# Kernel optimization log

Measured on AMD Instinct MI355X. Metric: run time of the kernel, lower is better.

The kernel has to match this reference:

```python
import jax, jax.numpy as jnp
import numpy as np

N_NODES = 100000
N_GRAPHS = 64
EPS = 1e-5


def _sage_conv(x, src, dst, Wl, bl, Wr):
    # mean-aggregate neighbor messages (src -> dst), then lin_l(agg) + lin_r(x)
    n = x.shape[0]
    deg = jax.ops.segment_sum(jnp.ones_like(dst, dtype=x.dtype), dst, num_segments=n)
    agg = jax.ops.segment_sum(x[src], dst, num_segments=n)  # [N, d]
    agg = agg / jnp.maximum(deg, 1.0)[:, None]
    return agg @ Wl + bl + x @ Wr


def _bn_relu(x, gamma, beta):
    mu = jnp.mean(x, axis=0)
    var = jnp.var(x, axis=0)
    return jax.nn.relu((x - mu) * jax.lax.rsqrt(var + EPS) * gamma + beta)


def setup_inputs() -> dict:
    key = jax.random.key(0)
    ks = jax.random.split(key, 16)
    E = 1600000
    x = jax.random.normal(ks[0], (N_NODES, 2), dtype=jnp.float32)
    edge_index = jax.random.randint(ks[1], (2, E), 0, N_NODES, dtype=jnp.int64)
    batch = jnp.sort(jax.random.randint(ks[2], (N_NODES,), 0, N_GRAPHS, dtype=jnp.int64))

    def lin(k, din, dout):
        s = 1.0 / np.sqrt(din)
        return jax.random.uniform(k, (din, dout), jnp.float32, -s, s)

    d = {"x": x, "edge_index": edge_index, "batch": batch}
    dims = [(2, 32), (32, 64), (64, 128)]
    for i, (din, dout) in enumerate(dims, 1):
        k1, k2 = jax.random.split(ks[2 + i])
        d[f"Wl{i}"] = lin(k1, din, dout)
        d[f"bl{i}"] = jnp.zeros((dout,), jnp.float32)
        d[f"Wr{i}"] = lin(k2, din, dout)
        d[f"g{i}"] = jnp.ones((dout,), jnp.float32)
        d[f"be{i}"] = jnp.zeros((dout,), jnp.float32)
    d["Wf1"] = lin(ks[10], 128, 64)
    d["bf1"] = jnp.zeros((64,), jnp.float32)
    d["Wf2"] = lin(ks[11], 64, 1)
    d["bf2"] = jnp.zeros((1,), jnp.float32)
    return d


def reference(x, edge_index, batch,
              Wl1, bl1, Wr1, g1, be1,
              Wl2, bl2, Wr2, g2, be2,
              Wl3, bl3, Wr3, g3, be3,
              Wf1, bf1, Wf2, bf2):
    src, dst = edge_index[0], edge_index[1]
    h = _bn_relu(_sage_conv(x, src, dst, Wl1, bl1, Wr1), g1, be1)
    h = _bn_relu(_sage_conv(h, src, dst, Wl2, bl2, Wr2), g2, be2)
    h = _bn_relu(_sage_conv(h, src, dst, Wl3, bl3, Wr3), g3, be3)
    # global mean pool over graphs
    cnt = jax.ops.segment_sum(jnp.ones_like(batch, dtype=h.dtype), batch, num_segments=N_GRAPHS)
    pooled = jax.ops.segment_sum(h, batch, num_segments=N_GRAPHS) / jnp.maximum(cnt, 1.0)[:, None]
    out = jax.nn.relu(pooled @ Wf1 + bf1)
    # dropout is identity in eval mode
    return out @ Wf2 + bf2
```

## Files before the change

### kernel.cpp

```cpp
#include <hip/hip_runtime.h>
#include <hip/hip_fp16.h>

#define N_NODES 100000
#define N_GRAPHS 64
#define BN_EPS 1e-5

#define NB 782
#define NC 49
#define PT1 4096
#define PT2 2048
#define BPC 16
#define CAP 3072

typedef _Float16 f16x8 __attribute__((ext_vector_type(8)));
typedef float f32x4 __attribute__((ext_vector_type(4)));

union F16x8u {
    f16x8 v;
    __half2 h2[4];
    uint4 u;
};

__device__ __forceinline__ float bfly64(float v) {
#pragma unroll
    for (int m = 1; m < 64; m <<= 1) v += __shfl_xor(v, m, 64);
    return v;
}

__device__ __forceinline__ unsigned pack_h2(float a, float b) {
    __half2 h = __floats2half2_rn(a, b);
    unsigned w;
    __builtin_memcpy(&w, &h, 4);
    return w;
}

__device__ __forceinline__ float2 unpack_h2(unsigned w) {
    __half2 h;
    __builtin_memcpy(&h, &w, 4);
    return __half22float2(h);
}

__global__ void hist_fine(const int* __restrict__ dst, int* __restrict__ bhist, int E) {
    __shared__ int h[NB];
    for (int i = threadIdx.x; i < NB; i += 256) h[i] = 0;
    __syncthreads();
    int stride = gridDim.x * 256;
    for (int e = blockIdx.x * 256 + threadIdx.x; e < E; e += stride) {
        int d = __builtin_nontemporal_load(dst + e);
        atomicAdd(&h[d >> 7], 1);
    }
    __syncthreads();
    for (int i = threadIdx.x; i < NB; i += 256)
        if (h[i]) atomicAdd(&bhist[i], h[i]);
}

__global__ void scan_buckets(const int* __restrict__ bhist, int* __restrict__ bo,
                             int* __restrict__ fcur, int* __restrict__ co,
                             int* __restrict__ ccur) {
    __shared__ int sh[1024];
    int t = threadIdx.x;
    sh[t] = (t < NB) ? bhist[t] : 0;
    __syncthreads();
    for (int st = 1; st < 1024; st <<= 1) {
        int v = (t >= st) ? sh[t - st] : 0;
        __syncthreads();
        sh[t] += v;
        __syncthreads();
    }
    int total = sh[NB - 1];
    if (t < NB) {
        int e = t ? sh[t - 1] : 0;
        bo[t] = e; fcur[t] = e;
    } else if (t < 784) {
        if (t == NB) bo[NB] = total;
        fcur[t] = total;
    }
    if (t < NC) {
        int i = t << 4;
        int e = i ? sh[i - 1] : 0;
        co[t] = e; ccur[t] = e;
    } else if (t == NC) {
        co[NC] = total;
    }
}

__global__ __launch_bounds__(256)
void part1(const int* __restrict__ dst, const int* __restrict__ src,
           int* __restrict__ ccur, int* __restrict__ cdst, int* __restrict__ csrc, int E) {
    __shared__ int ld[PT1], ls[PT1];
    __shared__ unsigned char lb[PT1];
    __shared__ int hist[NC], lbase[NC], gbase[NC];
    long long t0 = (long long)blockIdx.x * PT1;
    int n = (int)min((long long)PT1, (long long)E - t0);
    int tid = threadIdx.x;
    for (int i = tid; i < NC; i += 256) hist[i] = 0;
    __syncthreads();
    int d[PT1 / 256], s[PT1 / 256], c[PT1 / 256];
#pragma unroll
    for (int k = 0; k < PT1 / 256; ++k) {
        int li = k * 256 + tid;
        if (li < n) {
            d[k] = __builtin_nontemporal_load(dst + t0 + li);
            s[k] = __builtin_nontemporal_load(src + t0 + li);
            c[k] = d[k] >> 11;
            atomicAdd(&hist[c[k]], 1);
        }
    }
    __syncthreads();
    if (tid == 0) {
        int run = 0;
        for (int i = 0; i < NC; ++i) { lbase[i] = run; run += hist[i]; }
    }
    __syncthreads();
    if (tid < NC) gbase[tid] = atomicAdd(&ccur[tid], hist[tid]);
    __syncthreads();
    for (int i = tid; i < NC; i += 256) hist[i] = 0;
    __syncthreads();
#pragma unroll
    for (int k = 0; k < PT1 / 256; ++k) {
        int li = k * 256 + tid;
        if (li < n) {
            int pos = lbase[c[k]] + atomicAdd(&hist[c[k]], 1);
            ld[pos] = d[k]; ls[pos] = s[k]; lb[pos] = (unsigned char)c[k];
        }
    }
    __syncthreads();
    for (int i = tid; i < n; i += 256) {
        int bb = lb[i];
        int g = gbase[bb] + (i - lbase[bb]);
        cdst[g] = ld[i];
        csrc[g] = ls[i];
    }
}

__global__ __launch_bounds__(256)
void part2(const int* __restrict__ cdst, const int* __restrict__ csrc,
           const int* __restrict__ co, int* __restrict__ fcur,
           int* __restrict__ qdst, int* __restrict__ qsrc) {
    __shared__ int ld[PT2], ls[PT2];
    __shared__ unsigned char lb[PT2];
    __shared__ int hist[16], lbase[16], gbase[16];
    int c = blockIdx.x / BPC;
    int j = blockIdx.x % BPC;
    int beg = co[c], end = co[c + 1];
    int tid = threadIdx.x;
    for (int t0 = beg + j * PT2; t0 < end; t0 += BPC * PT2) {
        int n = min(PT2, end - t0);
        if (tid < 16) hist[tid] = 0;
        __syncthreads();
        int d[PT2 / 256], s[PT2 / 256], f[PT2 / 256];
#pragma unroll
        for (int k = 0; k < PT2 / 256; ++k) {
            int li = k * 256 + tid;
            if (li < n) {
                d[k] = cdst[t0 + li];
                s[k] = csrc[t0 + li];
                f[k] = (d[k] >> 7) & 15;
                atomicAdd(&hist[f[k]], 1);
            }
        }
        __syncthreads();
        if (tid == 0) {
            int run = 0;
            for (int i = 0; i < 16; ++i) { lbase[i] = run; run += hist[i]; }
        }
        __syncthreads();
        if (tid < 16) gbase[tid] = atomicAdd(&fcur[(c << 4) + tid], hist[tid]);
        __syncthreads();
        if (tid < 16) hist[tid] = 0;
        __syncthreads();
#pragma unroll
        for (int k = 0; k < PT2 / 256; ++k) {
            int li = k * 256 + tid;
            if (li < n) {
                int pos = lbase[f[k]] + atomicAdd(&hist[f[k]], 1);
                ld[pos] = d[k]; ls[pos] = s[k]; lb[pos] = (unsigned char)f[k];
            }
        }
        __syncthreads();
        for (int i = tid; i < n; i += 256) {
            int bb = lb[i];
            int g = gbase[bb] + (i - lbase[bb]);
            qdst[g] = ld[i];
            qsrc[g] = ls[i];
        }
        __syncthreads();
    }
}

__global__ __launch_bounds__(256)
void fill_final(const int* __restrict__ qdst, const int* __restrict__ qsrc,
                const int* __restrict__ bo, int* __restrict__ offs,
                int* __restrict__ nbr, int N, int E) {
    __shared__ int cnt[128], cbase[128], cur[128];
    __shared__ int lout[CAP];
    int b = blockIdx.x;
    int nlo = b << 7;
    int nn = min(128, N - nlo);
    int ebeg = bo[b], ne = bo[b + 1] - ebeg;
    int tid = threadIdx.x;
    if (tid < 128) { cnt[tid] = 0; cur[tid] = 0; }
    __syncthreads();
    for (int i = tid; i < ne; i += 256)
        atomicAdd(&cnt[qdst[ebeg + i] - nlo], 1);
    __syncthreads();
    if (tid < 128) cbase[tid] = cnt[tid];
    __syncthreads();
    for (int st = 1; st < 128; st <<= 1) {
        int v = 0;
        if (tid < 128 && tid >= st) v = cbase[tid - st];
        __syncthreads();
        if (tid < 128 && tid >= st) cbase[tid] += v;
        __syncthreads();
    }
    if (tid < nn)
        offs[nlo + tid] = ebeg + (tid ? cbase[tid - 1] : 0);
    if (b == NB - 1 && tid == 0) offs[N] = E;
    __syncthreads();
    for (int i = tid; i < ne; i += 256) {
        int d = qdst[ebeg + i];
        int s = qsrc[ebeg + i];
        int ln = d - nlo;
        int p = (ln ? cbase[ln - 1] : 0) + atomicAdd(&cur[ln], 1);
        lout[p] = s;
    }
    __syncthreads();
    for (int i = tid; i < ne; i += 256)
        nbr[ebeg + i] = lout[i];
}

__global__ __launch_bounds__(256)
void layer1_fused(const float2* __restrict__ x2,
                  const int* __restrict__ offs, const int* __restrict__ nbr,
                  const float* __restrict__ Wl, const float* __restrict__ bl,
                  const float* __restrict__ Wr,
                  __half* __restrict__ hout16,
                  double* __restrict__ sums, int N) {
    __shared__ float sAr[64];
    int tid = threadIdx.x;
    if (tid < 64) sAr[tid] = 0.f;
    __syncthreads();
    int n = blockIdx.x * 256 + tid;
    bool valid = (n < N);
    int beg = 0, end = 0;
    if (valid) { beg = offs[n]; end = offs[n + 1]; }
    double ax = 0.0, ay = 0.0;
    int j = beg;
    for (; j + 4 <= end; j += 4) {
        int s0 = nbr[j], s1 = nbr[j + 1], s2 = nbr[j + 2], s3 = nbr[j + 3];
        float2 v0 = x2[s0], v1 = x2[s1], v2 = x2[s2], v3 = x2[s3];
        ax += v0.x; ay += v0.y;
        ax += v1.x; ay += v1.y;
        ax += v2.x; ay += v2.y;
        ax += v3.x; ay += v3.y;
    }
    for (; j < end; ++j) {
        float2 v = x2[nbr[j]];
        ax += v.x; ay += v.y;
    }
    float invd = 1.0f / fmaxf((float)(end - beg), 1.0f);
    float a0 = (float)ax * invd, a1 = (float)ay * invd;
    float x0 = 0.f, x1 = 0.f;
    if (valid) {
        float2 xv = x2[n];
        x0 = xv.x; x1 = xv.y;
    }
    float acc[32];
#pragma unroll
    for (int jj = 0; jj < 32; ++jj)
        acc[jj] = bl[jj] + a0 * Wl[jj] + a1 * Wl[32 + jj] + x0 * Wr[jj] + x1 * Wr[32 + jj];
    if (valid) {
        unsigned w[16];
#pragma unroll
        for (int p = 0; p < 16; ++p) w[p] = pack_h2(acc[2*p], acc[2*p+1]);
        uint4* q = (uint4*)(hout16 + (size_t)n * 32);
        q[0] = make_uint4(w[0], w[1], w[2], w[3]);
        q[1] = make_uint4(w[4], w[5], w[6], w[7]);
        q[2] = make_uint4(w[8], w[9], w[10], w[11]);
        q[3] = make_uint4(w[12], w[13], w[14], w[15]);
    }
    int lane = tid & 63;
#pragma unroll
    for (int jj = 0; jj < 32; ++jj) {
        float v = valid ? acc[jj] : 0.f;
        float s = bfly64(v);
        float q = bfly64(v * v);
        if (lane == jj) atomicAdd(&sAr[jj], s);
        if (lane == 32 + jj) atomicAdd(&sAr[32 + jj], q);
    }
    __syncthreads();
    if (tid < 64) atomicAdd(&sums[tid], (double)sAr[tid]);
}

template<int F>
__global__ __launch_bounds__(256)
void agg_h16(const uint2* __restrict__ xh, const int* __restrict__ offs,
             const int* __restrict__ nbr,
             const double* __restrict__ sums,
             const float* __restrict__ gamma, const float* __restrict__ beta,
             uint2* __restrict__ aggh, int N) {
    constexpr int FV = F / 4;
    constexpr int NPB = 256 / FV;
    __shared__ float lsc[F], lsf[F];
    int tid = threadIdx.y * FV + threadIdx.x;
    if (tid < F) {
        double mu = sums[tid] / (double)N_NODES;
        double var = sums[F + tid] / (double)N_NODES - mu * mu;
        if (var < 0.0) var = 0.0;
        double sc = (double)gamma[tid] / sqrt(var + BN_EPS);
        lsc[tid] = (float)sc;
        lsf[tid] = (float)((double)beta[tid] - mu * sc);
    }
    __syncthreads();
    int n = blockIdx.x * NPB + threadIdx.y;
    if (n >= N) return;
    int f = threadIdx.x;
    float4 sc = ((const float4*)lsc)[f];
    float4 sf = ((const float4*)lsf)[f];
    int beg = offs[n], end = offs[n + 1];
    double ax = 0.0, ay = 0.0, az = 0.0, aw = 0.0;
    int j = beg;
    for (; j + 8 <= end; j += 8) {
        int s[8];
#pragma unroll
        for (int u = 0; u < 8; ++u) s[u] = __builtin_nontemporal_load(nbr + j + u);
        uint2 uv[8];
#pragma unroll
        for (int u = 0; u < 8; ++u) uv[u] = xh[(long long)s[u] * FV + f];
#pragma unroll
        for (int u = 0; u < 8; ++u) {
            float2 f0 = unpack_h2(uv[u].x);
            float2 f1 = unpack_h2(uv[u].y);
            ax += fmaxf(f0.x * sc.x + sf.x, 0.f);
            ay += fmaxf(f0.y * sc.y + sf.y, 0.f);
            az += fmaxf(f1.x * sc.z + sf.z, 0.f);
            aw += fmaxf(f1.y * sc.w + sf.w, 0.f);
        }
    }
    for (; j + 4 <= end; j += 4) {
        int s[4];
#pragma unroll
        for (int u = 0; u < 4; ++u) s[u] = __builtin_nontemporal_load(nbr + j + u);
        uint2 uv[4];
#pragma unroll
        for (int u = 0; u < 4; ++u) uv[u] = xh[(long long)s[u] * FV + f];
#pragma unroll
        for (int u = 0; u < 4; ++u) {
            float2 f0 = unpack_h2(uv[u].x);
            float2 f1 = unpack_h2(uv[u].y);
            ax += fmaxf(f0.x * sc.x + sf.x, 0.f);
            ay += fmaxf(f0.y * sc.y + sf.y, 0.f);
            az += fmaxf(f1.x * sc.z + sf.z, 0.f);
            aw += fmaxf(f1.y * sc.w + sf.w, 0.f);
        }
    }
    for (; j < end; ++j) {
        int s = __builtin_nontemporal_load(nbr + j);
        uint2 uv = xh[(long long)s * FV + f];
        float2 f0 = unpack_h2(uv.x);
        float2 f1 = unpack_h2(uv.y);
        ax += fmaxf(f0.x * sc.x + sf.x, 0.f);
        ay += fmaxf(f0.y * sc.y + sf.y, 0.f);
        az += fmaxf(f1.x * sc.z + sf.z, 0.f);
        aw += fmaxf(f1.y * sc.w + sf.w, 0.f);
    }
    uint2 out;
    out.x = pack_h2((float)ax, (float)ay);
    out.y = pack_h2((float)az, (float)aw);
    aggh[(long long)n * FV + f] = out;
}

__global__ __launch_bounds__(256)
void pack_w(const float* __restrict__ Wl2, const float* __restrict__ Wr2,
            const float* __restrict__ Wl3, const float* __restrict__ Wr3,
            __half* __restrict__ pk) {
    int e = blockIdx.x * 256 + threadIdx.x;
    const float* W; int le, DOUT, NCB, base, SZ;
    if (e < 2048)       { W = Wl2; le = e;         DOUT = 64;  NCB = 4; base = 0;     SZ = 2048; }
    else if (e < 4096)  { W = Wr2; le = e - 2048;  DOUT = 64;  NCB = 4; base = 4096;  SZ = 2048; }
    else if (e < 12288) { W = Wl3; le = e - 4096;  DOUT = 128; NCB = 8; base = 8192;  SZ = 8192; }
    else                { W = Wr3; le = e - 12288; DOUT = 128; NCB = 8; base = 24576; SZ = 8192; }
    int i = le & 7;
    int lane = (le >> 3) & 63;
    int cbkb = le >> 9;
    int cb = cbkb % NCB;
    int kb = cbkb / NCB;
    int k = kb * 32 + ((lane >> 4) << 3) + i;
    int col = cb * 16 + (lane & 15);
    float w = W[k * DOUT + col];
    __half h = __float2half(w);
    float lo = w - __half2float(h);
    pk[base + le] = h;
    pk[base + SZ + le] = __float2half(lo);
}

template<int DIN, int DOUT>
__global__ __launch_bounds__(256)
void linear_mfma(const __half* __restrict__ xin16, const __half* __restrict__ agg16,
                 const int* __restrict__ offs,
                 const __half* __restrict__ wlhi, const __half* __restrict__ wllo,
                 const __half* __restrict__ wrhi, const __half* __restrict__ wrlo,
                 const float* __restrict__ bl,
                 const double* __restrict__ sumsIn,
                 const float* __restrict__ gIn, const float* __restrict__ beIn,
                 __half* __restrict__ hout16, float* __restrict__ partial, int N) {
    constexpr int KB = DIN / 32;
    constexpr int NCB = DOUT / 16;
    constexpr int MREP = 2;
    constexpr int MB = 4 * MREP * 16;
    __shared__ float lsc[DIN], lsf[DIN];
    __shared__ float shInvd[MB];
    __shared__ float blkS[DOUT], blkQ[DOUT];
    int tid = threadIdx.x;
    if (tid < DIN) {
        double mu = sumsIn[tid] / (double)N_NODES;
        double var = sumsIn[DIN + tid] / (double)N_NODES - mu * mu;
        if (var < 0.0) var = 0.0;
        double sc = (double)gIn[tid] / sqrt(var + BN_EPS);
        lsc[tid] = (float)sc;
        lsf[tid] = (float)((double)beIn[tid] - mu * sc);
    }
    for (int i = tid; i < DOUT; i += 256) { blkS[i] = 0.f; blkQ[i] = 0.f; }
    int n0 = blockIdx.x * MB;
    for (int i = tid; i < MB; i += 256) {
        int nn = min(n0 + i, N - 1);
        shInvd[i] = 1.0f / fmaxf((float)(offs[nn + 1] - offs[nn]), 1.0f);
    }
    __syncthreads();

    int wave = tid >> 6;
    int lane = tid & 63;
    int rlane = lane & 15;
    int kg = lane >> 4;
    int rbase = n0 + wave * (MREP * 16);

    f16x8 aA[MREP][KB], aX[MREP][KB];
#pragma unroll
    for (int m = 0; m < MREP; ++m) {
        int row = rbase + m * 16 + rlane;
        int rowc = min(row, N - 1);
        float invd = shInvd[wave * (MREP * 16) + m * 16 + rlane];
#pragma unroll
        for (int kb = 0; kb < KB; ++kb) {
            int c0 = kb * 32 + kg * 8;
            F16x8u ta, tx;
            ta.u = *(const uint4*)(agg16 + (size_t)rowc * DIN + c0);
            tx.u = *(const uint4*)(xin16 + (size_t)rowc * DIN + c0);
#pragma unroll
            for (int q = 0; q < 4; ++q) {
                float2 fa = __half22float2(ta.h2[q]);
                ta.h2[q] = __floats2half2_rn(fa.x * invd, fa.y * invd);
                float2 fx = __half22float2(tx.h2[q]);
                int c = c0 + 2 * q;
                fx.x = fmaxf(fx.x * lsc[c] + lsf[c], 0.f);
                fx.y = fmaxf(fx.y * lsc[c + 1] + lsf[c + 1], 0.f);
                tx.h2[q] = __floats2half2_rn(fx.x, fx.y);
            }
            aA[m][kb] = ta.v;
            aX[m][kb] = tx.v;
        }
    }

    f32x4 acc[MREP][NCB];
#pragma unroll
    for (int cb = 0; cb < NCB; ++cb) {
        float bv = bl[cb * 16 + rlane];
#pragma unroll
        for (int m = 0; m < MREP; ++m)
            acc[m][cb] = {bv, bv, bv, bv};
    }

#pragma unroll
    for (int cb = 0; cb < NCB; ++cb) {
#pragma unroll
        for (int kb = 0; kb < KB; ++kb) {
            size_t fo = ((size_t)(kb * NCB + cb) * 64 + lane) * 8;
            f16x8 blh = *(const f16x8*)(wlhi + fo);
            f16x8 bll = *(const f16x8*)(wllo + fo);
            f16x8 brh = *(const f16x8*)(wrhi + fo);
            f16x8 brl = *(const f16x8*)(wrlo + fo);
#pragma unroll
            for (int m = 0; m < MREP; ++m) {
                acc[m][cb] = __builtin_amdgcn_mfma_f32_16x16x32_f16(aA[m][kb], blh, acc[m][cb], 0, 0, 0);
                acc[m][cb] = __builtin_amdgcn_mfma_f32_16x16x32_f16(aA[m][kb], bll, acc[m][cb], 0, 0, 0);
                acc[m][cb] = __builtin_amdgcn_mfma_f32_16x16x32_f16(aX[m][kb], brh, acc[m][cb], 0, 0, 0);
                acc[m][cb] = __builtin_amdgcn_mfma_f32_16x16x32_f16(aX[m][kb], brl, acc[m][cb], 0, 0, 0);
            }
        }
    }

#pragma unroll
    for (int m = 0; m < MREP; ++m) {
        int rowb = rbase + m * 16 + kg * 4;
#pragma unroll
        for (int r = 0; r < 4; ++r) {
            int node = rowb + r;
            if (node < N) {
#pragma unroll
                for (int cb = 0; cb < NCB; ++cb)
                    hout16[(size_t)node * DOUT + cb * 16 + rlane] = __float2half(acc[m][cb][r]);
            }
        }
    }

#pragma unroll
    for (int cb = 0; cb < NCB; ++cb) {
        float s = 0.f, q = 0.f;
#pragma unroll
        for (int m = 0; m < MREP; ++m) {
            int rowb = rbase + m * 16 + kg * 4;
#pragma unroll
            for (int r = 0; r < 4; ++r) {
                if (rowb + r < N) {
                    float v = acc[m][cb][r];
                    s += v; q += v * v;
                }
            }
        }
        s += __shfl_xor(s, 16, 64); s += __shfl_xor(s, 32, 64);
        q += __shfl_xor(q, 16, 64); q += __shfl_xor(q, 32, 64);
        if (kg == 0) {
            atomicAdd(&blkS[cb * 16 + rlane], s);
            atomicAdd(&blkQ[cb * 16 + rlane], q);
        }
    }
    __syncthreads();
    float* po = partial + (size_t)blockIdx.x * (2 * DOUT);
    for (int i = tid; i < DOUT; i += 256) {
        po[i] = blkS[i];
        po[DOUT + i] = blkQ[i];
    }
}

template<int F>
__global__ __launch_bounds__(256)
void stats_finalize2(const float* __restrict__ partial, double* __restrict__ sums, int P) {
    __shared__ double sh[256];
    int i = blockIdx.x;
    int t = threadIdx.x;
    double a = 0.0;
    for (int k = t; k < P; k += 256)
        a += (double)partial[(size_t)k * (2 * F) + i];
    sh[t] = a;
    __syncthreads();
    for (int st = 128; st > 0; st >>= 1) {
        if (t < st) sh[t] += sh[t + st];
        __syncthreads();
    }
    if (t == 0) sums[i] = sh[0];
}

__global__ void pool_partial(const __half* __restrict__ h, const int* __restrict__ batch,
                             const double* __restrict__ sums,
                             const float* __restrict__ gamma, const float* __restrict__ beta,
                             double* __restrict__ pooled_d, int N) {
    __shared__ float lsc[128], lsf[128];
    const int CH = 64;
    int f = threadIdx.x;
    {
        double mu = sums[f] / (double)N_NODES;
        double var = sums[128 + f] / (double)N_NODES - mu * mu;
        if (var < 0.0) var = 0.0;
        double sc = (double)gamma[f] / sqrt(var + BN_EPS);
        lsc[f] = (float)sc;
        lsf[f] = (float)((double)beta[f] - mu * sc);
    }
    __syncthreads();
    int n0 = blockIdx.x * CH;
    if (n0 >= N) return;
    int n1 = min(n0 + CH, N);
    float sc = lsc[f], sf = lsf[f];
    int g = batch[n0];
    float acc = 0.f;
    for (int n = n0; n < n1; ++n) {
        int bg = batch[n];
        if (bg != g) {
            atomicAdd(&pooled_d[g * 128 + f], (double)acc);
            acc = 0.f;
            g = bg;
        }
        float v = __half2float(h[(long long)n * 128 + f]);
        acc += fmaxf(v * sc + sf, 0.f);
    }
    atomicAdd(&pooled_d[g * 128 + f], (double)acc);
}

__global__ void mlp_fused(const double* __restrict__ pooled_d, const int* __restrict__ batch,
                          const float* __restrict__ Wf1, const float* __restrict__ bf1,
                          const float* __restrict__ Wf2, const float* __restrict__ bf2,
                          float* __restrict__ out, int N) {
    __shared__ float sp[128];
    int g = blockIdx.x;
    int t = threadIdx.x;
    int lo = 0, hi = N;
    while (lo < hi) { int m = (lo + hi) >> 1; if (batch[m] < g) lo = m + 1; else hi = m; }
    int start = lo;
    hi = N;
    while (lo < hi) { int m = (lo + hi) >> 1; if (batch[m] < g + 1) lo = m + 1; else hi = m; }
    int cnt = lo - start;
    sp[t] = (float)(pooled_d[g * 128 + t] / (double)max(cnt, 1));
    __syncthreads();
    if (t < 64) {
        float hacc = bf1[t];
#pragma unroll 8
        for (int k = 0; k < 128; ++k) hacc += sp[k] * Wf1[k * 64 + t];
        hacc = fmaxf(hacc, 0.f) * Wf2[t];
        for (int o = 32; o > 0; o >>= 1) hacc += __shfl_down(hacc, o);
        if (t == 0) out[g] = hacc + bf2[0];
    }
}

extern "C" void kernel_launch(void* const* d_in, const int* in_sizes, int n_in,
                              void* d_out, int out_size, void* d_ws, size_t ws_size,
                              hipStream_t stream) {
    const float* x     = (const float*)d_in[0];
    const int*   ei    = (const int*)d_in[1];
    const int*   batch = (const int*)d_in[2];
    const float *Wl1=(const float*)d_in[3],  *bl1=(const float*)d_in[4],  *Wr1=(const float*)d_in[5];
    const float *g1 =(const float*)d_in[6],  *be1=(const float*)d_in[7];
    const float *Wl2=(const float*)d_in[8],  *bl2=(const float*)d_in[9],  *Wr2=(const float*)d_in[10];
    const float *g2 =(const float*)d_in[11], *be2=(const float*)d_in[12];
    const float *Wl3=(const float*)d_in[13], *bl3=(const float*)d_in[14], *Wr3=(const float*)d_in[15];
    const float *g3 =(const float*)d_in[16], *be3=(const float*)d_in[17];
    const float *Wf1=(const float*)d_in[18], *bf1=(const float*)d_in[19];
    const float *Wf2=(const float*)d_in[20], *bf2=(const float*)d_in[21];

    const int N = N_NODES;
    const int E = in_sizes[1] / 2;
    const int* src = ei;
    const int* dst = ei + E;

    char* ws = (char*)d_ws;
    size_t off = 0;
    auto salloc = [&](size_t bytes) {
        void* p = ws + off;
        off += (bytes + 255) & ~(size_t)255;
        return p;
    };
    int*    bhist   = (int*)   salloc(NB * 4);
    double* sums    = (double*)salloc(768 * 8);
    double* pooledd = (double*)salloc((size_t)N_GRAPHS * 128 * 8);
    size_t zero_bytes = off;
    int*    offs    = (int*)   salloc((size_t)(N + 1) * 4);
    int*    bo      = (int*)   salloc((NB + 1) * 4);
    int*    fcur    = (int*)   salloc(784 * 4);
    int*    co      = (int*)   salloc((NC + 1) * 4);
    int*    ccur    = (int*)   salloc(NC * 4);
    int*    nbr     = (int*)   salloc((size_t)E * 4);
    float*  partial = (float*) salloc((size_t)1024 * 256 * 4);
    __half* pk      = (__half*)salloc((size_t)40960 * 2);
    __half* h1h     = (__half*)salloc((size_t)(N + 256) * 32 * 2);
    __half* h2h     = (__half*)salloc((size_t)(N + 256) * 64 * 2);
    __half* h3h     = (__half*)salloc((size_t)(N + 256) * 128 * 2);
    __half* aggh    = (__half*)salloc((size_t)(N + 256) * 64 * 2);
    (void)ws_size;

    double* sums1 = sums, *sums2 = sums + 256, *sums3 = sums + 512;
    int* cdst = (int*)h3h;
    int* csrc = cdst + E;
    int* qdst = (int*)aggh;
    int* qsrc = qdst + E;

    const __half *pwl2h = pk,         *pwl2l = pk + 2048;
    const __half *pwr2h = pk + 4096,  *pwr2l = pk + 6144;
    const __half *pwl3h = pk + 8192,  *pwl3l = pk + 16384;
    const __half *pwr3h = pk + 24576, *pwr3l = pk + 32768;

    hipMemsetAsync(bhist, 0, zero_bytes, stream);

    pack_w<<<80, 256, 0, stream>>>(Wl2, Wr2, Wl3, Wr3, pk);

    hist_fine<<<1024, 256, 0, stream>>>(dst, bhist, E);
    scan_buckets<<<1, 1024, 0, stream>>>(bhist, bo, fcur, co, ccur);
    part1<<<(E + PT1 - 1) / PT1, 256, 0, stream>>>(dst, src, ccur, cdst, csrc, E);
    part2<<<NC * BPC, 256, 0, stream>>>(cdst, csrc, co, fcur, qdst, qsrc);
    fill_final<<<NB, 256, 0, stream>>>(qdst, qsrc, bo, offs, nbr, N, E);

    const int NL = (N + 255) / 256;
    const int NBLK = (N + 127) / 128;

    layer1_fused<<<NL, 256, 0, stream>>>((const float2*)x, offs, nbr,
                                          Wl1, bl1, Wr1, h1h, sums1, N);

    agg_h16<32><<<(N + 31) / 32, dim3(8, 32), 0, stream>>>(
        (const uint2*)h1h, offs, nbr, sums1, g1, be1, (uint2*)aggh, N);
    linear_mfma<32, 64><<<NBLK, 256, 0, stream>>>(
        h1h, aggh, offs, pwl2h, pwl2l, pwr2h, pwr2l, bl2,
        sums1, g1, be1, h2h, partial, N);
    stats_finalize2<64><<<128, 256, 0, stream>>>(partial, sums2, NBLK);

    agg_h16<64><<<(N + 15) / 16, dim3(16, 16), 0, stream>>>(
        (const uint2*)h2h, offs, nbr, sums2, g2, be2, (uint2*)aggh, N);
    linear_mfma<64, 128><<<NBLK, 256, 0, stream>>>(
        h2h, aggh, offs, pwl3h, pwl3l, pwr3h, pwr3l, bl3,
        sums2, g2, be2, h3h, partial, N);
    stats_finalize2<128><<<256, 256, 0, stream>>>(partial, sums3, NBLK);

    pool_partial<<<(N + 63) / 64, 128, 0, stream>>>(h3h, batch, sums3, g3, be3, pooledd, N);
    mlp_fused<<<N_GRAPHS, 128, 0, stream>>>(pooledd, batch, Wf1, bf1, Wf2, bf2, (float*)d_out, N);
}
```

Before: 346.5 us.

## Materialize BN+ReLU once per node before neighbor aggregation, widen gathers to 16B

Batch-norm and ReLU are no longer applied to every gathered neighbor row inside the aggregation. A separate bn_apply pass now writes a normalized fp16 copy of each layer's activations, and a simpler agg_sum kernel sums those rows with 16-byte loads, float instead of double accumulators, and the mean division folded in. The linear MFMA kernel then reads the pre-normalized inputs and drops its own BN and inverse-degree work. This removes redundant per-edge arithmetic and the double-precision adds, at the cost of an extra kernel launch and an extra full read and write of the activations per layer.

```diff
diff --git a/kernel.cpp b/kernel.cpp
--- a/kernel.cpp
+++ b/kernel.cpp
@@ -294,15 +294,11 @@
 
 template<int F>
 __global__ __launch_bounds__(256)
-void agg_h16(const uint2* __restrict__ xh, const int* __restrict__ offs,
-             const int* __restrict__ nbr,
-             const double* __restrict__ sums,
-             const float* __restrict__ gamma, const float* __restrict__ beta,
-             uint2* __restrict__ aggh, int N) {
-    constexpr int FV = F / 4;
-    constexpr int NPB = 256 / FV;
-    __shared__ float lsc[F], lsf[F];
-    int tid = threadIdx.y * FV + threadIdx.x;
+void bn_apply(const uint4* __restrict__ h, const double* __restrict__ sums,
+              const float* __restrict__ gamma, const float* __restrict__ beta,
+              uint4* __restrict__ out, int N) {
+    __shared__ __align__(16) float lsc[F], lsf[F];
+    int tid = threadIdx.x;
     if (tid < F) {
         double mu = sums[tid] / (double)N_NODES;
         double var = sums[F + tid] / (double)N_NODES - mu * mu;
@@ -312,62 +308,71 @@
         lsf[tid] = (float)((double)beta[tid] - mu * sc);
     }
     __syncthreads();
+    constexpr int FV = F / 8;
+    int total = N * FV;
+    for (int i = blockIdx.x * 256 + tid; i < total; i += gridDim.x * 256) {
+        uint4 v = h[i];
+        int c4 = (i & (FV - 1)) * 2;
+        float4 sca = ((const float4*)lsc)[c4];
+        float4 scb = ((const float4*)lsc)[c4 + 1];
+        float4 sfa = ((const float4*)lsf)[c4];
+        float4 sfb = ((const float4*)lsf)[c4 + 1];
+        float2 f0 = unpack_h2(v.x), f1 = unpack_h2(v.y);
+        float2 f2 = unpack_h2(v.z), f3 = unpack_h2(v.w);
+        uint4 o;
+        o.x = pack_h2(fmaxf(f0.x * sca.x + sfa.x, 0.f), fmaxf(f0.y * sca.y + sfa.y, 0.f));
+        o.y = pack_h2(fmaxf(f1.x * sca.z + sfa.z, 0.f), fmaxf(f1.y * sca.w + sfa.w, 0.f));
+        o.z = pack_h2(fmaxf(f2.x * scb.x + sfb.x, 0.f), fmaxf(f2.y * scb.y + sfb.y, 0.f));
+        o.w = pack_h2(fmaxf(f3.x * scb.z + sfb.z, 0.f), fmaxf(f3.y * scb.w + sfb.w, 0.f));
+        out[i] = o;
+    }
+}
+
+template<int F>
+__global__ __launch_bounds__(256)
+void agg_sum(const uint4* __restrict__ xb, const int* __restrict__ offs,
+             const int* __restrict__ nbr, uint4* __restrict__ aggh, int N) {
+    constexpr int FV = F / 8;
+    constexpr int NPB = 256 / FV;
     int n = blockIdx.x * NPB + threadIdx.y;
     if (n >= N) return;
     int f = threadIdx.x;
-    float4 sc = ((const float4*)lsc)[f];
-    float4 sf = ((const float4*)lsf)[f];
     int beg = offs[n], end = offs[n + 1];
-    double ax = 0.0, ay = 0.0, az = 0.0, aw = 0.0;
+    float a0[8], a1[8];
+#pragma unroll
+    for (int q = 0; q < 8; ++q) { a0[q] = 0.f; a1[q] = 0.f; }
     int j = beg;
     for (; j + 8 <= end; j += 8) {
         int s[8];
 #pragma unroll
         for (int u = 0; u < 8; ++u) s[u] = __builtin_nontemporal_load(nbr + j + u);
-        uint2 uv[8];
-#pragma unroll
-        for (int u = 0; u < 8; ++u) uv[u] = xh[(long long)s[u] * FV + f];
+        uint4 v[8];
+#pragma unroll
+        for (int u = 0; u < 8; ++u) v[u] = xb[s[u] * FV + f];
 #pragma unroll
         for (int u = 0; u < 8; ++u) {
-            float2 f0 = unpack_h2(uv[u].x);
-            float2 f1 = unpack_h2(uv[u].y);
-            ax += fmaxf(f0.x * sc.x + sf.x, 0.f);
-            ay += fmaxf(f0.y * sc.y + sf.y, 0.f);
-            az += fmaxf(f1.x * sc.z + sf.z, 0.f);
-            aw += fmaxf(f1.y * sc.w + sf.w, 0.f);
-        }
-    }
-    for (; j + 4 <= end; j += 4) {
-        int s[4];
-#pragma unroll
-        for (int u = 0; u < 4; ++u) s[u] = __builtin_nontemporal_load(nbr + j + u);
-        uint2 uv[4];
-#pragma unroll
-        for (int u = 0; u < 4; ++u) uv[u] = xh[(long long)s[u] * FV + f];
-#pragma unroll
-        for (int u = 0; u < 4; ++u) {
-            float2 f0 = unpack_h2(uv[u].x);
-            float2 f1 = unpack_h2(uv[u].y);
-            ax += fmaxf(f0.x * sc.x + sf.x, 0.f);
-            ay += fmaxf(f0.y * sc.y + sf.y, 0.f);
-            az += fmaxf(f1.x * sc.z + sf.z, 0.f);
-            aw += fmaxf(f1.y * sc.w + sf.w, 0.f);
+            float* acc = (u & 1) ? a1 : a0;
+            float2 f0 = unpack_h2(v[u].x), f1 = unpack_h2(v[u].y);
+            float2 f2 = unpack_h2(v[u].z), f3 = unpack_h2(v[u].w);
+            acc[0] += f0.x; acc[1] += f0.y; acc[2] += f1.x; acc[3] += f1.y;
+            acc[4] += f2.x; acc[5] += f2.y; acc[6] += f3.x; acc[7] += f3.y;
         }
     }
     for (; j < end; ++j) {
         int s = __builtin_nontemporal_load(nbr + j);
-        uint2 uv = xh[(long long)s * FV + f];
-        float2 f0 = unpack_h2(uv.x);
-        float2 f1 = unpack_h2(uv.y);
-        ax += fmaxf(f0.x * sc.x + sf.x, 0.f);
-        ay += fmaxf(f0.y * sc.y + sf.y, 0.f);
-        az += fmaxf(f1.x * sc.z + sf.z, 0.f);
-        aw += fmaxf(f1.y * sc.w + sf.w, 0.f);
-    }
-    uint2 out;
-    out.x = pack_h2((float)ax, (float)ay);
-    out.y = pack_h2((float)az, (float)aw);
-    aggh[(long long)n * FV + f] = out;
+        uint4 v = xb[s * FV + f];
+        float2 f0 = unpack_h2(v.x), f1 = unpack_h2(v.y);
+        float2 f2 = unpack_h2(v.z), f3 = unpack_h2(v.w);
+        a0[0] += f0.x; a0[1] += f0.y; a0[2] += f1.x; a0[3] += f1.y;
+        a0[4] += f2.x; a0[5] += f2.y; a0[6] += f3.x; a0[7] += f3.y;
+    }
+    float invd = 1.0f / fmaxf((float)(end - beg), 1.0f);
+    uint4 o;
+    o.x = pack_h2((a0[0] + a1[0]) * invd, (a0[1] + a1[1]) * invd);
+    o.y = pack_h2((a0[2] + a1[2]) * invd, (a0[3] + a1[3]) * invd);
+    o.z = pack_h2((a0[4] + a1[4]) * invd, (a0[5] + a1[5]) * invd);
+    o.w = pack_h2((a0[6] + a1[6]) * invd, (a0[7] + a1[7]) * invd);
+    aggh[n * FV + f] = o;
 }
 
 __global__ __launch_bounds__(256)
@@ -396,37 +401,20 @@
 
 template<int DIN, int DOUT>
 __global__ __launch_bounds__(256)
-void linear_mfma(const __half* __restrict__ xin16, const __half* __restrict__ agg16,
-                 const int* __restrict__ offs,
+void linear_mfma(const __half* __restrict__ bnx16, const __half* __restrict__ agg16,
                  const __half* __restrict__ wlhi, const __half* __restrict__ wllo,
                  const __half* __restrict__ wrhi, const __half* __restrict__ wrlo,
                  const float* __restrict__ bl,
-                 const double* __restrict__ sumsIn,
-                 const float* __restrict__ gIn, const float* __restrict__ beIn,
                  __half* __restrict__ hout16, float* __restrict__ partial, int N) {
     constexpr int KB = DIN / 32;
     constexpr int NCB = DOUT / 16;
     constexpr int MREP = 2;
     constexpr int MB = 4 * MREP * 16;
-    __shared__ float lsc[DIN], lsf[DIN];
-    __shared__ float shInvd[MB];
     __shared__ float blkS[DOUT], blkQ[DOUT];
     int tid = threadIdx.x;
-    if (tid < DIN) {
-        double mu = sumsIn[tid] / (double)N_NODES;
-        double var = sumsIn[DIN + tid] / (double)N_NODES - mu * mu;
-        if (var < 0.0) var = 0.0;
-        double sc = (double)gIn[tid] / sqrt(var + BN_EPS);
-        lsc[tid] = (float)sc;
-        lsf[tid] = (float)((double)beIn[tid] - mu * sc);
-    }
     for (int i = tid; i < DOUT; i += 256) { blkS[i] = 0.f; blkQ[i] = 0.f; }
+    __syncthreads();
     int n0 = blockIdx.x * MB;
-    for (int i = tid; i < MB; i += 256) {
-        int nn = min(n0 + i, N - 1);
-        shInvd[i] = 1.0f / fmaxf((float)(offs[nn + 1] - offs[nn]), 1.0f);
-    }
-    __syncthreads();
 
     int wave = tid >> 6;
     int lane = tid & 63;
@@ -439,23 +427,12 @@
     for (int m = 0; m < MREP; ++m) {
         int row = rbase + m * 16 + rlane;
         int rowc = min(row, N - 1);
-        float invd = shInvd[wave * (MREP * 16) + m * 16 + rlane];
 #pragma unroll
         for (int kb = 0; kb < KB; ++kb) {
             int c0 = kb * 32 + kg * 8;
             F16x8u ta, tx;
             ta.u = *(const uint4*)(agg16 + (size_t)rowc * DIN + c0);
-            tx.u = *(const uint4*)(xin16 + (size_t)rowc * DIN + c0);
-#pragma unroll
-            for (int q = 0; q < 4; ++q) {
-                float2 fa = __half22float2(ta.h2[q]);
-                ta.h2[q] = __floats2half2_rn(fa.x * invd, fa.y * invd);
-                float2 fx = __half22float2(tx.h2[q]);
-                int c = c0 + 2 * q;
-                fx.x = fmaxf(fx.x * lsc[c] + lsf[c], 0.f);
-                fx.y = fmaxf(fx.y * lsc[c + 1] + lsf[c + 1], 0.f);
-                tx.h2[q] = __floats2half2_rn(fx.x, fx.y);
-            }
+            tx.u = *(const uint4*)(bnx16 + (size_t)rowc * DIN + c0);
             aA[m][kb] = ta.v;
             aX[m][kb] = tx.v;
         }
@@ -650,7 +627,9 @@
     float*  partial = (float*) salloc((size_t)1024 * 256 * 4);
     __half* pk      = (__half*)salloc((size_t)40960 * 2);
     __half* h1h     = (__half*)salloc((size_t)(N + 256) * 32 * 2);
+    __half* b1h     = (__half*)salloc((size_t)(N + 256) * 32 * 2);
     __half* h2h     = (__half*)salloc((size_t)(N + 256) * 64 * 2);
+    __half* b2h     = (__half*)salloc((size_t)(N + 256) * 64 * 2);
     __half* h3h     = (__half*)salloc((size_t)(N + 256) * 128 * 2);
     __half* aggh    = (__half*)salloc((size_t)(N + 256) * 64 * 2);
     (void)ws_size;
@@ -682,18 +661,18 @@
     layer1_fused<<<NL, 256, 0, stream>>>((const float2*)x, offs, nbr,
                                           Wl1, bl1, Wr1, h1h, sums1, N);
 
-    agg_h16<32><<<(N + 31) / 32, dim3(8, 32), 0, stream>>>(
-        (const uint2*)h1h, offs, nbr, sums1, g1, be1, (uint2*)aggh, N);
+    bn_apply<32><<<512, 256, 0, stream>>>((const uint4*)h1h, sums1, g1, be1, (uint4*)b1h, N);
+    agg_sum<32><<<(N + 63) / 64, dim3(4, 64), 0, stream>>>(
+        (const uint4*)b1h, offs, nbr, (uint4*)aggh, N);
     linear_mfma<32, 64><<<NBLK, 256, 0, stream>>>(
-        h1h, aggh, offs, pwl2h, pwl2l, pwr2h, pwr2l, bl2,
-        sums1, g1, be1, h2h, partial, N);
+        b1h, (const __half*)aggh, pwl2h, pwl2l, pwr2h, pwr2l, bl2, h2h, partial, N);
     stats_finalize2<64><<<128, 256, 0, stream>>>(partial, sums2, NBLK);
 
-    agg_h16<64><<<(N + 15) / 16, dim3(16, 16), 0, stream>>>(
-        (const uint2*)h2h, offs, nbr, sums2, g2, be2, (uint2*)aggh, N);
+    bn_apply<64><<<512, 256, 0, stream>>>((const uint4*)h2h, sums2, g2, be2, (uint4*)b2h, N);
+    agg_sum<64><<<(N + 31) / 32, dim3(8, 32), 0, stream>>>(
+        (const uint4*)b2h, offs, nbr, (uint4*)aggh, N);
     linear_mfma<64, 128><<<NBLK, 256, 0, stream>>>(
-        h2h, aggh, offs, pwl3h, pwl3l, pwr3h, pwr3l, bl3,
-        sums2, g2, be2, h3h, partial, N);
+        b2h, (const __half*)aggh, pwl3h, pwl3l, pwr3h, pwr3l, bl3, h3h, partial, N);
     stats_finalize2<128><<<256, 256, 0, stream>>>(partial, sums3, NBLK);
 
     pool_partial<<<(N + 63) / 64, 128, 0, stream>>>(h3h, batch, sums3, g3, be3, pooledd, N);
```

Measured after the change: 347.6 us. No clear change (+0.3%).
